# Kernel optimization log

Hardware: AMD Instinct MI355X
Metric: run time of the kernel (lower is better)

Reference implementation:

```python
import jax, jax.numpy as jnp
import numpy as np

B, N, D, H, DH, E, BIAS_DIM = 8, 512, 512, 8, 64, 32768, 8

def setup_inputs() -> dict:
    key = jax.random.key(0)
    ks = jax.random.split(key, 10)
    states = jax.random.normal(ks[0], (B, N, D), jnp.float32)
    key_states = jax.random.normal(ks[1], (B, N, D), jnp.float32)
    # causal mask, broadcastable over heads: [B,1,N,N]
    masks = jnp.broadcast_to(jnp.tril(jnp.ones((N, N), jnp.float32)), (B, 1, N, N))
    edge_type = jax.random.randint(ks[2], (E, 1), 0, BIAS_DIM, jnp.int32)
    b_idx = jax.random.randint(ks[3], (E, 1), 0, B, jnp.int32)
    q_idx = jax.random.randint(ks[4], (E, 1), 0, N, jnp.int32)
    k_idx = jax.random.randint(ks[5], (E, 1), 0, N, jnp.int32)
    attention_bias = jnp.concatenate([edge_type, b_idx, q_idx, k_idx], axis=1)
    s = 0.05
    Wq = jax.random.normal(ks[6], (D, H, DH), jnp.float32) * s
    Wk = jax.random.normal(ks[7], (D, H, DH), jnp.float32) * s
    Wv = jax.random.normal(ks[8], (D, H, DH), jnp.float32) * s
    k2 = jax.random.split(ks[9], 3)
    Wo = jax.random.normal(k2[0], (H, DH, D), jnp.float32) * s
    bias_embs = jax.random.normal(k2[1], (BIAS_DIM, DH), jnp.float32) * s
    bias_scalar = jax.random.normal(k2[2], (DH, 1), jnp.float32) * s
    return {"states": states, "key_states": key_states, "masks": masks,
            "attention_bias": attention_bias, "Wq": Wq, "Wk": Wk, "Wv": Wv,
            "Wo": Wo, "bias_embs": bias_embs, "bias_scalar": bias_scalar}

def reference(states, key_states, masks, attention_bias, Wq, Wk, Wv, Wo, bias_embs, bias_scalar):
    q = jnp.einsum('btd,dha->btha', states, Wq)
    k = jnp.einsum('btd,dha->btha', key_states, Wk)
    v = jnp.einsum('btd,dha->btha', key_states, Wv)
    alpha = jnp.einsum('bkha,bqha->bhqk', k, q)  # [B,H,Q,K]
    # sparse edge bias: embed edge types, project to scalar, scatter into [B,Q,K]
    et = attention_bias[:, 0]
    bias_vals = (bias_embs[et] @ bias_scalar)[:, 0]  # [E]
    bq, bk = alpha.shape[2], alpha.shape[3]
    bias_mat = jnp.zeros((alpha.shape[0], bq, bk), alpha.dtype)
    bias_mat = bias_mat.at[attention_bias[:, 1], attention_bias[:, 2], attention_bias[:, 3]].add(bias_vals)
    summed_keys = jnp.sum(k, axis=-1)  # [B,K,H]
    alpha = alpha + jnp.einsum('bqk,bkh->bhqk', bias_mat, summed_keys)
    alpha = alpha * jax.lax.rsqrt(jnp.float32(DH))
    neg = jnp.finfo(jnp.float32).min
    alpha = alpha * masks + (1.0 - jnp.ceil(masks)) * neg
    alpha = jax.nn.softmax(alpha, axis=-1)
    alpha = alpha * masks
    context = jnp.einsum('bhqk,bkha->bqha', alpha, v)
    return jnp.einsum('btha,had->btd', context, Wo)
```

## Files before the change

### kernel.cpp

```cpp
#include <hip/hip_runtime.h>

typedef unsigned short u16;
typedef unsigned int u32;
typedef __bf16 bf16x8 __attribute__((ext_vector_type(8)));
typedef float f32x4 __attribute__((ext_vector_type(4)));
typedef u16 u16x8 __attribute__((ext_vector_type(8)));
typedef u16 u16x4 __attribute__((ext_vector_type(4)));


__device__ __forceinline__ u16 f2b(float f) {
  union { float f; u32 i; } v; v.f = f;
  u32 r = v.i + 0x7fffu + ((v.i >> 16) & 1u);
  return (u16)(r >> 16);
}
__device__ __forceinline__ float b2f(u16 u) {
  union { u32 i; float f; } v; v.i = ((u32)u) << 16; return v.f;
}

#define GLL16(gp, lp)                                                      \
  __builtin_amdgcn_global_load_lds(                                       \
      (const __attribute__((address_space(1))) u32*)(gp),                 \
      (__attribute__((address_space(3))) u32*)(lp), 16, 0, 0)

__device__ __forceinline__ void stage64(const u16* g, u16* l, int wave, int lane) {
  int rsub = lane >> 3;
  int gs = (((lane & 7) ^ rsub) << 3);
  #pragma unroll
  for (int c = 0; c < 2; c++) {
    int ch = wave * 2 + c;
    GLL16(g + (size_t)(ch * 8 + rsub) * 512 + gs, l + ch * 512);
  }
}
__device__ __forceinline__ void stage128(const u16* g, u16* l, int wave, int lane) {
  int rsub = lane >> 3;
  int gs = (((lane & 7) ^ rsub) << 3);
  #pragma unroll
  for (int c = 0; c < 4; c++) {
    int ch = wave * 4 + c;
    GLL16(g + (size_t)(ch * 8 + rsub) * 512 + gs, l + ch * 512);
  }
}
__device__ __forceinline__ int swz(int row, int g) {
  return row * 64 + ((g ^ (row & 7)) << 3);
}

__global__ __launch_bounds__(256) void prologue(
    const float* __restrict__ states, const float* __restrict__ key_states,
    const float* __restrict__ Wq, const float* __restrict__ Wk,
    const float* __restrict__ Wv, const float* __restrict__ Wo,
    const int* __restrict__ ab, const float* __restrict__ be,
    const float* __restrict__ bsc,
    u16* __restrict__ sb, u16* __restrict__ kbin, u16* __restrict__ wbase,
    float* __restrict__ bias_mat, int n_edges) {
  __shared__ u16 t[32][33];
  __shared__ float tv[8];
  int bid = blockIdx.x;
  int tid = threadIdx.x;
  if (bid < 2048) {
    const float* src = (bid >= 1024) ? key_states : states;
    u16* dst = (bid >= 1024) ? kbin : sb;
    int gid = (bid & 1023) * 256 + tid;
    const float4* sp = (const float4*)src + (size_t)gid * 2;
    float4 x0 = sp[0], x1 = sp[1];
    u16x8 p;
    p[0] = f2b(x0.x); p[1] = f2b(x0.y); p[2] = f2b(x0.z); p[3] = f2b(x0.w);
    p[4] = f2b(x1.x); p[5] = f2b(x1.y); p[6] = f2b(x1.z); p[7] = f2b(x1.w);
    *(u16x8*)(dst + (size_t)gid * 8) = p;
  } else if (bid < 3072) {
    int tt = bid - 2048;
    int z = tt >> 8, rem = tt & 255;
    int bx = rem & 15, by = rem >> 4;
    const float* src; float sc = 1.f;
    if (z == 0)      { src = Wq; sc = 0.125f; }
    else if (z == 1) { src = Wk; }
    else if (z == 2) { src = Wv; }
    else             { src = Wo; }
    u16* dst = wbase + (size_t)z * 262144;
    int tx = tid & 31, ty = tid >> 5;
    int c0 = bx * 32, r0 = by * 32;
    #pragma unroll
    for (int i = ty; i < 32; i += 8) t[i][tx] = f2b(src[(r0 + i) * 512 + c0 + tx] * sc);
    __syncthreads();
    #pragma unroll
    for (int i = ty; i < 32; i += 8) dst[(c0 + i) * 512 + r0 + tx] = t[tx][i];
  } else {
    if (tid < 8) {
      float s = 0.f;
      #pragma unroll
      for (int a = 0; a < 64; a++) s += be[tid * 64 + a] * bsc[a];
      tv[tid] = s * 0.125f;
    }
    __syncthreads();
    int e = (bid - 3072) * 256 + tid;
    if (e < n_edges) {
      int et = ab[e * 4 + 0];
      int b  = ab[e * 4 + 1];
      int qi = ab[e * 4 + 2];
      int ki = ab[e * 4 + 3];
      atomicAdd(&bias_mat[((size_t)b * 512 + qi) * 512 + ki], tv[et]);
    }
  }
}

__global__ __launch_bounds__(256) void qkv_gemm(const u16* __restrict__ sb,
                                                const u16* __restrict__ kbin,
                                                const u16* __restrict__ wT,
                                                u16* __restrict__ qb,
                                                u16* __restrict__ kbo,
                                                u16* __restrict__ vtb,
                                                float* __restrict__ summed) {
  __shared__ alignas(16) u16 As[2][64 * 64];
  __shared__ alignas(16) u16 Bs[2][128 * 64];
  __shared__ float ssum[4][64];
  int tid = threadIdx.x;
  int lane = tid & 63, wave = tid >> 6;
  int quad = lane >> 4, ln = lane & 15;
  int row0 = blockIdx.x * 64;
  int col0 = blockIdx.y * 128;
  const u16* A = (col0 < 512) ? sb : kbin;
  const u16* Ab = A + (size_t)row0 * 512;
  const u16* Bb = wT + (size_t)col0 * 512;

  f32x4 acc[4][2];
  #pragma unroll
  for (int i = 0; i < 4; i++)
    #pragma unroll
    for (int j = 0; j < 2; j++) acc[i][j] = (f32x4){0.f, 0.f, 0.f, 0.f};

  stage64(Ab, As[0], wave, lane);
  stage128(Bb, Bs[0], wave, lane);

  int cur = 0;
  for (int k0 = 0; k0 < 512; k0 += 64) {
    __syncthreads();
    if (k0 < 448) {
      stage64(Ab + k0 + 64, As[cur ^ 1], wave, lane);
      stage128(Bb + k0 + 64, Bs[cur ^ 1], wave, lane);
    }
    #pragma unroll
    for (int s = 0; s < 2; s++) {
      bf16x8 af[4], bfv[2];
      #pragma unroll
      for (int i = 0; i < 4; i++)
        af[i] = *(bf16x8*)&As[cur][swz(i * 16 + ln, s * 4 + quad)];
      #pragma unroll
      for (int j = 0; j < 2; j++)
        bfv[j] = *(bf16x8*)&Bs[cur][swz(wave * 32 + j * 16 + ln, s * 4 + quad)];
      #pragma unroll
      for (int i = 0; i < 4; i++)
        #pragma unroll
        for (int j = 0; j < 2; j++)
          acc[i][j] = __builtin_amdgcn_mfma_f32_16x16x32_bf16(af[i], bfv[j], acc[i][j], 0, 0, 0);
    }
    cur ^= 1;
  }

  int region = col0 >> 9;
  int nbase = col0 & 511;
  if (region <= 1) {
    u16* Cout = region ? kbo : qb;
    #pragma unroll
    for (int i = 0; i < 4; i++)
      #pragma unroll
      for (int j = 0; j < 2; j++) {
        int mb = row0 + i * 16 + quad * 4;
        int n = nbase + wave * 32 + j * 16 + ln;
        #pragma unroll
        for (int r = 0; r < 4; r++)
          Cout[(size_t)(mb + r) * 512 + n] = f2b(acc[i][j][r]);
      }
    if (region == 1) {
      #pragma unroll
      for (int i = 0; i < 4; i++)
        #pragma unroll
        for (int r = 0; r < 4; r++) {
          float v = acc[i][0][r] + acc[i][1][r];
          v += __shfl_xor(v, 1);
          v += __shfl_xor(v, 2);
          v += __shfl_xor(v, 4);
          v += __shfl_xor(v, 8);
          if (ln == 0) ssum[wave][i * 16 + quad * 4 + r] = v;
        }
      __syncthreads();
      if (tid < 128) {
        int hl = tid >> 6, row = tid & 63;
        float s = ssum[hl * 2][row] + ssum[hl * 2 + 1][row];
        int m = row0 + row;
        int b = m >> 9, t = m & 511;
        int h = (nbase >> 6) + hl;
        summed[((size_t)(b * 8 + h)) * 512 + t] = s;
      }
    }
  } else {
    #pragma unroll
    for (int i = 0; i < 4; i++)
      #pragma unroll
      for (int j = 0; j < 2; j++) {
        int mb = row0 + i * 16 + quad * 4;
        int bb = mb >> 9, t0 = mb & 511;
        int a_abs = nbase + wave * 32 + j * 16 + ln;
        int h = a_abs >> 6, a = a_abs & 63;
        u16x4 p;
        p[0] = f2b(acc[i][j][0]); p[1] = f2b(acc[i][j][1]);
        p[2] = f2b(acc[i][j][2]); p[3] = f2b(acc[i][j][3]);
        *(u16x4*)&vtb[(((size_t)bb * 8 + h) * 64 + a) * 512 + t0] = p;
      }
  }
}

__global__ __launch_bounds__(256) void out_gemm(const u16* __restrict__ A,
                                                const u16* __restrict__ BT,
                                                float* __restrict__ C) {
  __shared__ alignas(16) u16 As[2][64 * 64];
  __shared__ alignas(16) u16 Bs[2][64 * 64];
  int tid = threadIdx.x;
  int lane = tid & 63, wave = tid >> 6;
  int quad = lane >> 4, ln = lane & 15;
  int wr = wave >> 1, wc = wave & 1;
  int row0 = blockIdx.x * 64;
  int col0 = blockIdx.y * 64;
  const u16* Ab = A + (size_t)row0 * 512;
  const u16* Bb = BT + (size_t)col0 * 512;

  f32x4 acc[2][2];
  #pragma unroll
  for (int i = 0; i < 2; i++)
    #pragma unroll
    for (int j = 0; j < 2; j++) acc[i][j] = (f32x4){0.f, 0.f, 0.f, 0.f};

  stage64(Ab, As[0], wave, lane);
  stage64(Bb, Bs[0], wave, lane);

  int cur = 0;
  for (int k0 = 0; k0 < 512; k0 += 64) {
    __syncthreads();
    if (k0 < 448) {
      stage64(Ab + k0 + 64, As[cur ^ 1], wave, lane);
      stage64(Bb + k0 + 64, Bs[cur ^ 1], wave, lane);
    }
    #pragma unroll
    for (int s = 0; s < 2; s++) {
      bf16x8 af[2], bfv[2];
      #pragma unroll
      for (int i = 0; i < 2; i++)
        af[i] = *(bf16x8*)&As[cur][swz(wr * 32 + i * 16 + ln, s * 4 + quad)];
      #pragma unroll
      for (int j = 0; j < 2; j++)
        bfv[j] = *(bf16x8*)&Bs[cur][swz(wc * 32 + j * 16 + ln, s * 4 + quad)];
      #pragma unroll
      for (int i = 0; i < 2; i++)
        #pragma unroll
        for (int j = 0; j < 2; j++)
          acc[i][j] = __builtin_amdgcn_mfma_f32_16x16x32_bf16(af[i], bfv[j], acc[i][j], 0, 0, 0);
    }
    cur ^= 1;
  }
  #pragma unroll
  for (int i = 0; i < 2; i++)
    #pragma unroll
    for (int j = 0; j < 2; j++) {
      int mb = row0 + wr * 32 + i * 16 + quad * 4;
      int n = col0 + wc * 32 + j * 16 + ln;
      #pragma unroll
      for (int r = 0; r < 4; r++)
        C[(size_t)(mb + r) * 512 + n] = acc[i][j][r];
    }
}

__global__ __launch_bounds__(256) void attn_mfma(const u16* __restrict__ q,
                                                 const u16* __restrict__ k,
                                                 const u16* __restrict__ vt,
                                                 const float* __restrict__ bias_mat,
                                                 const float* __restrict__ summed,
                                                 u16* __restrict__ ctx,
                                                 float* __restrict__ Opart,
                                                 float* __restrict__ ml) {
  __shared__ alignas(16) u16 Qs[64 * 64];
  __shared__ alignas(16) u16 Ks[2][64 * 64];
  __shared__ alignas(16) u16 Vs[2][64 * 64];
  __shared__ alignas(16) u16 Ps[4][16 * 72];
  int tid = threadIdx.x;
  int wave = tid >> 6, lane = tid & 63;
  int quad = lane >> 4, ln = lane & 15;
  int p2 = blockIdx.x;
  int bh, u;
  {
    const int fours[6] = {3, 4, 6, 8, 10, 11};
    const int threes[2] = {2, 9};
    const int ones[2] = {0, 5};
    const int twos[2] = {1, 7};
    if (p2 < 384)      { bh = p2 & 63; u = fours[p2 >> 6]; }
    else if (p2 < 512) { int q2 = p2 - 384; bh = q2 & 63; u = threes[q2 >> 6]; }
    else if (p2 < 640) { int q2 = p2 - 512; bh = q2 & 63; u = ones[q2 >> 6]; }
    else               { int q2 = p2 - 640; bh = q2 & 63; u = twos[q2 >> 6]; }
  }
  int b = bh >> 3, h = bh & 7;
  int qt, kb0, kbe, part = 0;
  bool partial;
  if (u < 4) { qt = u; kb0 = 0; kbe = u; partial = false; }
  else {
    int v = u - 4; qt = 4 + (v >> 1); part = v & 1; partial = true;
    if (part == 0) { kb0 = 0; kbe = 3; } else { kb0 = 4; kbe = qt; }
  }
  int q0 = qt * 64;

  const u16* qb_ = q + ((size_t)(b * 512 + q0)) * 512 + h * 64;
  const u16* kb_ = k + ((size_t)(b * 512)) * 512 + h * 64;
  const u16* vb_ = vt + ((size_t)bh * 64) * 512;

  stage64(qb_, Qs, wave, lane);
  stage64(kb_ + (size_t)kb0 * 64 * 512, Ks[0], wave, lane);
  stage64(vb_ + kb0 * 64, Vs[0], wave, lane);

  float m_r[4], l_r[4];
  f32x4 o[4];
  #pragma unroll
  for (int r = 0; r < 4; r++) { m_r[r] = -3.40282347e38f; l_r[r] = 0.f; }
  #pragma unroll
  for (int nt = 0; nt < 4; nt++) o[nt] = (f32x4){0.f, 0.f, 0.f, 0.f};

  int qrow = q0 + wave * 16 + quad * 4;

  float c_skv[4], c_bias[4][4];
  #pragma unroll
  for (int nt = 0; nt < 4; nt++) {
    int t = kb0 * 64 + nt * 16 + ln;
    c_skv[nt] = summed[bh * 512 + t];
    const float* bp2 = bias_mat + ((size_t)(b * 512 + qrow)) * 512 + t;
    #pragma unroll
    for (int r = 0; r < 4; r++) c_bias[nt][r] = bp2[(size_t)r * 512];
  }

  int cur = 0;
  for (int kb = kb0; kb <= kbe; kb++) {
    __syncthreads();

    float n_skv[4], n_bias[4][4];
    if (kb < kbe) {
      stage64(kb_ + (size_t)(kb + 1) * 64 * 512, Ks[cur ^ 1], wave, lane);
      stage64(vb_ + (kb + 1) * 64, Vs[cur ^ 1], wave, lane);
      #pragma unroll
      for (int nt = 0; nt < 4; nt++) {
        int t = (kb + 1) * 64 + nt * 16 + ln;
        n_skv[nt] = summed[bh * 512 + t];
        const float* bp2 = bias_mat + ((size_t)(b * 512 + qrow)) * 512 + t;
        #pragma unroll
        for (int r = 0; r < 4; r++) n_bias[nt][r] = bp2[(size_t)r * 512];
      }
    }

    bf16x8 aq0 = *(bf16x8*)&Qs[swz(wave * 16 + ln, quad)];
    bf16x8 aq1 = *(bf16x8*)&Qs[swz(wave * 16 + ln, 4 + quad)];
    f32x4 s[4];
    #pragma unroll
    for (int nt = 0; nt < 4; nt++) {
      bf16x8 b0 = *(bf16x8*)&Ks[cur][swz(nt * 16 + ln, quad)];
      bf16x8 b1 = *(bf16x8*)&Ks[cur][swz(nt * 16 + ln, 4 + quad)];
      s[nt] = (f32x4){0.f, 0.f, 0.f, 0.f};
      s[nt] = __builtin_amdgcn_mfma_f32_16x16x32_bf16(aq0, b0, s[nt], 0, 0, 0);
      s[nt] = __builtin_amdgcn_mfma_f32_16x16x32_bf16(aq1, b1, s[nt], 0, 0, 0);
    }

    #pragma unroll
    for (int nt = 0; nt < 4; nt++) {
      int t = kb * 64 + nt * 16 + ln;
      #pragma unroll
      for (int r = 0; r < 4; r++) {
        float val = s[nt][r] + c_bias[nt][r] * c_skv[nt];
        s[nt][r] = (t <= qrow + r) ? val : -3.40282347e38f;
      }
    }

    float alpha[4];
    #pragma unroll
    for (int r = 0; r < 4; r++) {
      float tm = fmaxf(fmaxf(s[0][r], s[1][r]), fmaxf(s[2][r], s[3][r]));
      #pragma unroll
      for (int off = 8; off; off >>= 1) tm = fmaxf(tm, __shfl_xor(tm, off));
      float mn = fmaxf(m_r[r], tm);
      alpha[r] = __expf(m_r[r] - mn);
      m_r[r] = mn;
      float rs = 0.f;
      #pragma unroll
      for (int nt = 0; nt < 4; nt++) {
        float pp = __expf(s[nt][r] - mn);
        s[nt][r] = pp;
        rs += pp;
      }
      #pragma unroll
      for (int off = 8; off; off >>= 1) rs += __shfl_xor(rs, off);
      l_r[r] = l_r[r] * alpha[r] + rs;
    }

    #pragma unroll
    for (int nt = 0; nt < 4; nt++)
      #pragma unroll
      for (int r = 0; r < 4; r++)
        Ps[wave][(quad * 4 + r) * 72 + nt * 16 + ln] = f2b(s[nt][r]);
    #pragma unroll
    for (int nt = 0; nt < 4; nt++)
      #pragma unroll
      for (int r = 0; r < 4; r++)
        o[nt][r] *= alpha[r];

    bf16x8 ap0 = *(bf16x8*)&Ps[wave][ln * 72 + quad * 8];
    bf16x8 ap1 = *(bf16x8*)&Ps[wave][ln * 72 + 32 + quad * 8];
    #pragma unroll
    for (int nt = 0; nt < 4; nt++) {
      bf16x8 b0 = *(bf16x8*)&Vs[cur][swz(nt * 16 + ln, quad)];
      bf16x8 b1 = *(bf16x8*)&Vs[cur][swz(nt * 16 + ln, 4 + quad)];
      o[nt] = __builtin_amdgcn_mfma_f32_16x16x32_bf16(ap0, b0, o[nt], 0, 0, 0);
      o[nt] = __builtin_amdgcn_mfma_f32_16x16x32_bf16(ap1, b1, o[nt], 0, 0, 0);
    }

    if (kb < kbe) {
      #pragma unroll
      for (int nt = 0; nt < 4; nt++) {
        c_skv[nt] = n_skv[nt];
        #pragma unroll
        for (int r = 0; r < 4; r++) c_bias[nt][r] = n_bias[nt][r];
      }
    }
    cur ^= 1;
  }

  if (!partial) {
    #pragma unroll
    for (int r = 0; r < 4; r++) {
      float inv = 1.f / l_r[r];
      int qr2 = qrow + r;
      u16* dst = ctx + ((size_t)(b * 512 + qr2)) * 512 + h * 64;
      #pragma unroll
      for (int nt = 0; nt < 4; nt++)
        dst[nt * 16 + ln] = f2b(o[nt][r] * inv);
    }
  } else {
    #pragma unroll
    for (int r = 0; r < 4; r++) {
      int row = qrow + r - 256;
      float* dst = Opart + (((size_t)(part * 64 + bh)) * 256 + row) * 64;
      #pragma unroll
      for (int nt = 0; nt < 4; nt++)
        dst[nt * 16 + ln] = o[nt][r];
    }
    if (ln == 0) {
      #pragma unroll
      for (int r = 0; r < 4; r++) {
        int row = qrow + r - 256;
        float* mp = ml + (((size_t)(part * 64 + bh)) * 256 + row) * 2;
        mp[0] = m_r[r];
        mp[1] = l_r[r];
      }
    }
  }
}

__global__ __launch_bounds__(256) void attn_merge(const float* __restrict__ Opart,
                                                  const float* __restrict__ ml,
                                                  u16* __restrict__ ctx) {
  int gid = blockIdx.x * 256 + threadIdx.x;
  int col = gid & 63;
  int row = (gid >> 6) & 255;
  int bh = gid >> 14;
  size_t i0 = (size_t)bh * 256 + row;
  size_t i1 = (size_t)(64 + bh) * 256 + row;
  float m0 = ml[i0 * 2], l0 = ml[i0 * 2 + 1];
  float m1 = ml[i1 * 2], l1 = ml[i1 * 2 + 1];
  float m = fmaxf(m0, m1);
  float a0 = __expf(m0 - m), a1 = __expf(m1 - m);
  float l = l0 * a0 + l1 * a1;
  float O0 = Opart[i0 * 64 + col], O1 = Opart[i1 * 64 + col];
  float val = (O0 * a0 + O1 * a1) / l;
  int b = bh >> 3, h = bh & 7, qrow = 256 + row;
  ctx[((size_t)(b * 512 + qrow)) * 512 + h * 64 + col] = f2b(val);
}

extern "C" void kernel_launch(void* const* d_in, const int* in_sizes, int n_in,
                              void* d_out, int out_size, void* d_ws, size_t ws_size,
                              hipStream_t stream) {
  const float* states     = (const float*)d_in[0];
  const float* key_states = (const float*)d_in[1];
  const int*   ab         = (const int*)d_in[3];
  const float* Wq         = (const float*)d_in[4];
  const float* Wk         = (const float*)d_in[5];
  const float* Wv         = (const float*)d_in[6];
  const float* Wo         = (const float*)d_in[7];
  const float* be         = (const float*)d_in[8];
  const float* bsc        = (const float*)d_in[9];
  float* out = (float*)d_out;

  char* ws = (char*)d_ws;
  const size_t MB = 1024 * 1024;
  u16* wbase    = (u16*)(ws);
  u16* wot      = (u16*)(ws + 1536 * 1024);
  u16* sb       = (u16*)(ws + 2 * MB);
  u16* kbin     = (u16*)(ws + 6 * MB);
  u16* qb       = (u16*)(ws + 10 * MB);
  u16* kbo      = (u16*)(ws + 14 * MB);
  u16* vtb      = (u16*)(ws + 18 * MB);
  u16* ctxb     = (u16*)(ws + 22 * MB);
  float* bias_m = (float*)(ws + 26 * MB);
  float* summed = (float*)(ws + 34 * MB);
  float* Opart  = (float*)(ws + 35 * MB);
  float* mlbuf  = (float*)(ws + 43 * MB);

  int n_edges = in_sizes[3] / 4;

  hipMemsetAsync(bias_m, 0, (size_t)8 * MB, stream);
  prologue<<<dim3(3072 + (n_edges + 255) / 256), 256, 0, stream>>>(
      states, key_states, Wq, Wk, Wv, Wo, ab, be, bsc, sb, kbin, wbase, bias_m, n_edges);
  qkv_gemm<<<dim3(64, 12), 256, 0, stream>>>(sb, kbin, wbase, qb, kbo, vtb, summed);
  attn_mfma<<<dim3(768), 256, 0, stream>>>(qb, kbo, vtb, bias_m, summed, ctxb, Opart, mlbuf);
  attn_merge<<<dim3(4096), 256, 0, stream>>>(Opart, mlbuf, ctxb);
  out_gemm<<<dim3(64, 8), 256, 0, stream>>>(ctxb, wot, out);
}
```

Measured before the change: 134.6 us.

## Fuse all stages into one persistent cooperative kernel with grid syncs

Replaces the memset plus five separate kernel launches with a single cooperative persistent kernel. Stages are separated by grid-wide barriers and use a shared-memory union. The bias zeroing and per-edge bias scalar computation move inside the kernel, and the edge scatter is deferred until after the barrier. This removes launch gaps and inter-kernel drain, at the cost of grid-sync overhead, grid-stride loops bounded by occupancy, and a larger shared-memory footprint that may lower occupancy.

```diff
diff --git a/kernel.cpp b/kernel.cpp
--- a/kernel.cpp
+++ b/kernel.cpp
@@ -1,4 +1,7 @@
 #include <hip/hip_runtime.h>
+#include <hip/hip_cooperative_groups.h>
+
+namespace cg = cooperative_groups;
 
 typedef unsigned short u16;
 typedef unsigned int u32;
@@ -12,9 +15,6 @@
   union { float f; u32 i; } v; v.f = f;
   u32 r = v.i + 0x7fffu + ((v.i >> 16) & 1u);
   return (u16)(r >> 16);
-}
-__device__ __forceinline__ float b2f(u16 u) {
-  union { u32 i; float f; } v; v.i = ((u32)u) << 16; return v.f;
 }
 
 #define GLL16(gp, lp)                                                      \
@@ -44,435 +44,439 @@
   return row * 64 + ((g ^ (row & 7)) << 3);
 }
 
-__global__ __launch_bounds__(256) void prologue(
+__global__ __launch_bounds__(256) void fused(
     const float* __restrict__ states, const float* __restrict__ key_states,
-    const float* __restrict__ Wq, const float* __restrict__ Wk,
-    const float* __restrict__ Wv, const float* __restrict__ Wo,
-    const int* __restrict__ ab, const float* __restrict__ be,
+    const int* __restrict__ ab, const float* __restrict__ Wq,
+    const float* __restrict__ Wk, const float* __restrict__ Wv,
+    const float* __restrict__ Wo, const float* __restrict__ be,
     const float* __restrict__ bsc,
     u16* __restrict__ sb, u16* __restrict__ kbin, u16* __restrict__ wbase,
-    float* __restrict__ bias_mat, int n_edges) {
-  __shared__ u16 t[32][33];
-  __shared__ float tv[8];
+    float* __restrict__ bias_m, float* __restrict__ summed,
+    u16* __restrict__ qb, u16* __restrict__ kbo, u16* __restrict__ vtb,
+    u16* __restrict__ ctxb, float* __restrict__ Opart, float* __restrict__ mlbuf,
+    float* __restrict__ out, int n_edges) {
+  __shared__ alignas(16) union SM {
+    u16 t[32][33];
+    struct {
+      alignas(16) u16 As[2][64 * 64];
+      alignas(16) u16 Bs[2][128 * 64];
+      float ssum[4][64];
+    } g1;
+    struct {
+      alignas(16) u16 Qs[64 * 64];
+      alignas(16) u16 Ks[2][64 * 64];
+      alignas(16) u16 Vs[2][64 * 64];
+      alignas(16) u16 Ps[4][16 * 72];
+    } at;
+    struct {
+      alignas(16) u16 As[2][64 * 64];
+      alignas(16) u16 Bs[2][64 * 64];
+    } g2;
+  } sm;
+
+  cg::grid_group gg = cg::this_grid();
+
+  int tid = threadIdx.x;
   int bid = blockIdx.x;
-  int tid = threadIdx.x;
-  if (bid < 2048) {
-    const float* src = (bid >= 1024) ? key_states : states;
-    u16* dst = (bid >= 1024) ? kbin : sb;
-    int gid = (bid & 1023) * 256 + tid;
-    const float4* sp = (const float4*)src + (size_t)gid * 2;
-    float4 x0 = sp[0], x1 = sp[1];
-    u16x8 p;
-    p[0] = f2b(x0.x); p[1] = f2b(x0.y); p[2] = f2b(x0.z); p[3] = f2b(x0.w);
-    p[4] = f2b(x1.x); p[5] = f2b(x1.y); p[6] = f2b(x1.z); p[7] = f2b(x1.w);
-    *(u16x8*)(dst + (size_t)gid * 8) = p;
-  } else if (bid < 3072) {
-    int tt = bid - 2048;
-    int z = tt >> 8, rem = tt & 255;
-    int bx = rem & 15, by = rem >> 4;
-    const float* src; float sc = 1.f;
-    if (z == 0)      { src = Wq; sc = 0.125f; }
-    else if (z == 1) { src = Wk; }
-    else if (z == 2) { src = Wv; }
-    else             { src = Wo; }
-    u16* dst = wbase + (size_t)z * 262144;
+  const int G = gridDim.x;
+  const int gsz = G << 8;
+  int gtid = bid * 256 + tid;
+  int lane = tid & 63, wave = tid >> 6;
+  int quad = lane >> 4, ln = lane & 15;
+
+  {
+    float4 z4 = {0.f, 0.f, 0.f, 0.f};
+    for (int i = gtid; i < 524288; i += gsz) ((float4*)bias_m)[i] = z4;
+
+    for (int c = gtid; c < 524288; c += gsz) {
+      const float* src = (c < 262144) ? states : key_states;
+      u16* dst = (c < 262144) ? sb : kbin;
+      int g = c & 262143;
+      const float4* sp = (const float4*)src + (size_t)g * 2;
+      float4 x0 = sp[0], x1 = sp[1];
+      u16x8 p;
+      p[0] = f2b(x0.x); p[1] = f2b(x0.y); p[2] = f2b(x0.z); p[3] = f2b(x0.w);
+      p[4] = f2b(x1.x); p[5] = f2b(x1.y); p[6] = f2b(x1.z); p[7] = f2b(x1.w);
+      *(u16x8*)(dst + (size_t)g * 8) = p;
+    }
+
     int tx = tid & 31, ty = tid >> 5;
-    int c0 = bx * 32, r0 = by * 32;
-    #pragma unroll
-    for (int i = ty; i < 32; i += 8) t[i][tx] = f2b(src[(r0 + i) * 512 + c0 + tx] * sc);
-    __syncthreads();
-    #pragma unroll
-    for (int i = ty; i < 32; i += 8) dst[(c0 + i) * 512 + r0 + tx] = t[tx][i];
-  } else {
-    if (tid < 8) {
-      float s = 0.f;
-      #pragma unroll
-      for (int a = 0; a < 64; a++) s += be[tid * 64 + a] * bsc[a];
-      tv[tid] = s * 0.125f;
-    }
-    __syncthreads();
-    int e = (bid - 3072) * 256 + tid;
-    if (e < n_edges) {
+    for (int tt = bid; tt < 1024; tt += G) {
+      int z = tt >> 8, rem = tt & 255;
+      int bx = rem & 15, by = rem >> 4;
+      const float* src; float sc = 1.f;
+      if (z == 0)      { src = Wq; sc = 0.125f; }
+      else if (z == 1) { src = Wk; }
+      else if (z == 2) { src = Wv; }
+      else             { src = Wo; }
+      u16* dst = wbase + (size_t)z * 262144;
+      int c0 = bx * 32, r0 = by * 32;
+      #pragma unroll
+      for (int i = ty; i < 32; i += 8) sm.t[i][tx] = f2b(src[(r0 + i) * 512 + c0 + tx] * sc);
+      __syncthreads();
+      #pragma unroll
+      for (int i = ty; i < 32; i += 8) dst[(c0 + i) * 512 + r0 + tx] = sm.t[tx][i];
+      __syncthreads();
+    }
+  }
+  gg.sync();
+
+  {
+    for (int e = gtid; e < n_edges; e += gsz) {
       int et = ab[e * 4 + 0];
       int b  = ab[e * 4 + 1];
       int qi = ab[e * 4 + 2];
       int ki = ab[e * 4 + 3];
-      atomicAdd(&bias_mat[((size_t)b * 512 + qi) * 512 + ki], tv[et]);
-    }
-  }
-}
-
-__global__ __launch_bounds__(256) void qkv_gemm(const u16* __restrict__ sb,
-                                                const u16* __restrict__ kbin,
-                                                const u16* __restrict__ wT,
-                                                u16* __restrict__ qb,
-                                                u16* __restrict__ kbo,
-                                                u16* __restrict__ vtb,
-                                                float* __restrict__ summed) {
-  __shared__ alignas(16) u16 As[2][64 * 64];
-  __shared__ alignas(16) u16 Bs[2][128 * 64];
-  __shared__ float ssum[4][64];
-  int tid = threadIdx.x;
-  int lane = tid & 63, wave = tid >> 6;
-  int quad = lane >> 4, ln = lane & 15;
-  int row0 = blockIdx.x * 64;
-  int col0 = blockIdx.y * 128;
-  const u16* A = (col0 < 512) ? sb : kbin;
-  const u16* Ab = A + (size_t)row0 * 512;
-  const u16* Bb = wT + (size_t)col0 * 512;
-
-  f32x4 acc[4][2];
-  #pragma unroll
-  for (int i = 0; i < 4; i++)
+      float s = 0.f;
+      #pragma unroll 8
+      for (int a = 0; a < 64; a++) s += be[et * 64 + a] * bsc[a];
+      atomicAdd(&bias_m[((size_t)b * 512 + qi) * 512 + ki], s * 0.125f);
+    }
+
+    for (int vb = bid; vb < 768; vb += G) {
+      __syncthreads();
+      int bx = vb & 63, by = vb >> 6;
+      int row0 = bx * 64;
+      int col0 = by * 128;
+      const u16* A = (col0 < 512) ? sb : kbin;
+      const u16* Ab = A + (size_t)row0 * 512;
+      const u16* Bb = wbase + (size_t)col0 * 512;
+
+      f32x4 acc[4][2];
+      #pragma unroll
+      for (int i = 0; i < 4; i++)
+        #pragma unroll
+        for (int j = 0; j < 2; j++) acc[i][j] = (f32x4){0.f, 0.f, 0.f, 0.f};
+
+      stage64(Ab, sm.g1.As[0], wave, lane);
+      stage128(Bb, sm.g1.Bs[0], wave, lane);
+
+      int cur = 0;
+      for (int k0 = 0; k0 < 512; k0 += 64) {
+        __syncthreads();
+        if (k0 < 448) {
+          stage64(Ab + k0 + 64, sm.g1.As[cur ^ 1], wave, lane);
+          stage128(Bb + k0 + 64, sm.g1.Bs[cur ^ 1], wave, lane);
+        }
+        #pragma unroll
+        for (int s = 0; s < 2; s++) {
+          bf16x8 af[4], bfv[2];
+          #pragma unroll
+          for (int i = 0; i < 4; i++)
+            af[i] = *(bf16x8*)&sm.g1.As[cur][swz(i * 16 + ln, s * 4 + quad)];
+          #pragma unroll
+          for (int j = 0; j < 2; j++)
+            bfv[j] = *(bf16x8*)&sm.g1.Bs[cur][swz(wave * 32 + j * 16 + ln, s * 4 + quad)];
+          #pragma unroll
+          for (int i = 0; i < 4; i++)
+            #pragma unroll
+            for (int j = 0; j < 2; j++)
+              acc[i][j] = __builtin_amdgcn_mfma_f32_16x16x32_bf16(af[i], bfv[j], acc[i][j], 0, 0, 0);
+        }
+        cur ^= 1;
+      }
+
+      int region = col0 >> 9;
+      int nbase = col0 & 511;
+      if (region <= 1) {
+        u16* Cout = region ? kbo : qb;
+        #pragma unroll
+        for (int i = 0; i < 4; i++)
+          #pragma unroll
+          for (int j = 0; j < 2; j++) {
+            int mb = row0 + i * 16 + quad * 4;
+            int n = nbase + wave * 32 + j * 16 + ln;
+            #pragma unroll
+            for (int r = 0; r < 4; r++)
+              Cout[(size_t)(mb + r) * 512 + n] = f2b(acc[i][j][r]);
+          }
+        if (region == 1) {
+          #pragma unroll
+          for (int i = 0; i < 4; i++)
+            #pragma unroll
+            for (int r = 0; r < 4; r++) {
+              float v = acc[i][0][r] + acc[i][1][r];
+              v += __shfl_xor(v, 1);
+              v += __shfl_xor(v, 2);
+              v += __shfl_xor(v, 4);
+              v += __shfl_xor(v, 8);
+              if (ln == 0) sm.g1.ssum[wave][i * 16 + quad * 4 + r] = v;
+            }
+          __syncthreads();
+          if (tid < 128) {
+            int hl = tid >> 6, row = tid & 63;
+            float s = sm.g1.ssum[hl * 2][row] + sm.g1.ssum[hl * 2 + 1][row];
+            int m = row0 + row;
+            int b = m >> 9, t = m & 511;
+            int h = (nbase >> 6) + hl;
+            summed[((size_t)(b * 8 + h)) * 512 + t] = s;
+          }
+        }
+      } else {
+        #pragma unroll
+        for (int i = 0; i < 4; i++)
+          #pragma unroll
+          for (int j = 0; j < 2; j++) {
+            int mb = row0 + i * 16 + quad * 4;
+            int bb = mb >> 9, t0 = mb & 511;
+            int a_abs = nbase + wave * 32 + j * 16 + ln;
+            int h = a_abs >> 6, a = a_abs & 63;
+            u16x4 p;
+            p[0] = f2b(acc[i][j][0]); p[1] = f2b(acc[i][j][1]);
+            p[2] = f2b(acc[i][j][2]); p[3] = f2b(acc[i][j][3]);
+            *(u16x4*)&vtb[(((size_t)bb * 8 + h) * 64 + a) * 512 + t0] = p;
+          }
+      }
+    }
+  }
+  gg.sync();
+
+  for (int vb = bid; vb < 768; vb += G) {
+    __syncthreads();
+    int p2 = vb;
+    int bh, u;
+    {
+      const int fours[6] = {3, 4, 6, 8, 10, 11};
+      const int threes[2] = {2, 9};
+      const int ones[2] = {0, 5};
+      const int twos[2] = {1, 7};
+      if (p2 < 384)      { bh = p2 & 63; u = fours[p2 >> 6]; }
+      else if (p2 < 512) { int q2 = p2 - 384; bh = q2 & 63; u = threes[q2 >> 6]; }
+      else if (p2 < 640) { int q2 = p2 - 512; bh = q2 & 63; u = ones[q2 >> 6]; }
+      else               { int q2 = p2 - 640; bh = q2 & 63; u = twos[q2 >> 6]; }
+    }
+    int b = bh >> 3, h = bh & 7;
+    int qt, kb0, kbe, part = 0;
+    bool partial;
+    if (u < 4) { qt = u; kb0 = 0; kbe = u; partial = false; }
+    else {
+      int v = u - 4; qt = 4 + (v >> 1); part = v & 1; partial = true;
+      if (part == 0) { kb0 = 0; kbe = 3; } else { kb0 = 4; kbe = qt; }
+    }
+    int q0 = qt * 64;
+
+    const u16* qb_ = qb + ((size_t)(b * 512 + q0)) * 512 + h * 64;
+    const u16* kb_ = kbo + ((size_t)(b * 512)) * 512 + h * 64;
+    const u16* vb_ = vtb + ((size_t)bh * 64) * 512;
+
+    stage64(qb_, sm.at.Qs, wave, lane);
+    stage64(kb_ + (size_t)kb0 * 64 * 512, sm.at.Ks[0], wave, lane);
+    stage64(vb_ + kb0 * 64, sm.at.Vs[0], wave, lane);
+
+    float m_r[4], l_r[4];
+    f32x4 o[4];
     #pragma unroll
-    for (int j = 0; j < 2; j++) acc[i][j] = (f32x4){0.f, 0.f, 0.f, 0.f};
-
-  stage64(Ab, As[0], wave, lane);
-  stage128(Bb, Bs[0], wave, lane);
-
-  int cur = 0;
-  for (int k0 = 0; k0 < 512; k0 += 64) {
-    __syncthreads();
-    if (k0 < 448) {
-      stage64(Ab + k0 + 64, As[cur ^ 1], wave, lane);
-      stage128(Bb + k0 + 64, Bs[cur ^ 1], wave, lane);
-    }
+    for (int r = 0; r < 4; r++) { m_r[r] = -3.40282347e38f; l_r[r] = 0.f; }
     #pragma unroll
-    for (int s = 0; s < 2; s++) {
-      bf16x8 af[4], bfv[2];
-      #pragma unroll
-      for (int i = 0; i < 4; i++)
-        af[i] = *(bf16x8*)&As[cur][swz(i * 16 + ln, s * 4 + quad)];
-      #pragma unroll
-      for (int j = 0; j < 2; j++)
-        bfv[j] = *(bf16x8*)&Bs[cur][swz(wave * 32 + j * 16 + ln, s * 4 + quad)];
-      #pragma unroll
-      for (int i = 0; i < 4; i++)
-        #pragma unroll
-        for (int j = 0; j < 2; j++)
-          acc[i][j] = __builtin_amdgcn_mfma_f32_16x16x32_bf16(af[i], bfv[j], acc[i][j], 0, 0, 0);
-    }
-    cur ^= 1;
-  }
-
-  int region = col0 >> 9;
-  int nbase = col0 & 511;
-  if (region <= 1) {
-    u16* Cout = region ? kbo : qb;
-    #pragma unroll
-    for (int i = 0; i < 4; i++)
-      #pragma unroll
-      for (int j = 0; j < 2; j++) {
-        int mb = row0 + i * 16 + quad * 4;
-        int n = nbase + wave * 32 + j * 16 + ln;
-        #pragma unroll
-        for (int r = 0; r < 4; r++)
-          Cout[(size_t)(mb + r) * 512 + n] = f2b(acc[i][j][r]);
-      }
-    if (region == 1) {
-      #pragma unroll
-      for (int i = 0; i < 4; i++)
-        #pragma unroll
-        for (int r = 0; r < 4; r++) {
-          float v = acc[i][0][r] + acc[i][1][r];
-          v += __shfl_xor(v, 1);
-          v += __shfl_xor(v, 2);
-          v += __shfl_xor(v, 4);
-          v += __shfl_xor(v, 8);
-          if (ln == 0) ssum[wave][i * 16 + quad * 4 + r] = v;
-        }
-      __syncthreads();
-      if (tid < 128) {
-        int hl = tid >> 6, row = tid & 63;
-        float s = ssum[hl * 2][row] + ssum[hl * 2 + 1][row];
-        int m = row0 + row;
-        int b = m >> 9, t = m & 511;
-        int h = (nbase >> 6) + hl;
-        summed[((size_t)(b * 8 + h)) * 512 + t] = s;
-      }
-    }
-  } else {
-    #pragma unroll
-    for (int i = 0; i < 4; i++)
-      #pragma unroll
-      for (int j = 0; j < 2; j++) {
-        int mb = row0 + i * 16 + quad * 4;
-        int bb = mb >> 9, t0 = mb & 511;
-        int a_abs = nbase + wave * 32 + j * 16 + ln;
-        int h = a_abs >> 6, a = a_abs & 63;
-        u16x4 p;
-        p[0] = f2b(acc[i][j][0]); p[1] = f2b(acc[i][j][1]);
-        p[2] = f2b(acc[i][j][2]); p[3] = f2b(acc[i][j][3]);
-        *(u16x4*)&vtb[(((size_t)bb * 8 + h) * 64 + a) * 512 + t0] = p;
-      }
-  }
-}
-
-__global__ __launch_bounds__(256) void out_gemm(const u16* __restrict__ A,
-                                                const u16* __restrict__ BT,
-                                                float* __restrict__ C) {
-  __shared__ alignas(16) u16 As[2][64 * 64];
-  __shared__ alignas(16) u16 Bs[2][64 * 64];
-  int tid = threadIdx.x;
-  int lane = tid & 63, wave = tid >> 6;
-  int quad = lane >> 4, ln = lane & 15;
-  int wr = wave >> 1, wc = wave & 1;
-  int row0 = blockIdx.x * 64;
-  int col0 = blockIdx.y * 64;
-  const u16* Ab = A + (size_t)row0 * 512;
-  const u16* Bb = BT + (size_t)col0 * 512;
-
-  f32x4 acc[2][2];
-  #pragma unroll
-  for (int i = 0; i < 2; i++)
-    #pragma unroll
-    for (int j = 0; j < 2; j++) acc[i][j] = (f32x4){0.f, 0.f, 0.f, 0.f};
-
-  stage64(Ab, As[0], wave, lane);
-  stage64(Bb, Bs[0], wave, lane);
-
-  int cur = 0;
-  for (int k0 = 0; k0 < 512; k0 += 64) {
-    __syncthreads();
-    if (k0 < 448) {
-      stage64(Ab + k0 + 64, As[cur ^ 1], wave, lane);
-      stage64(Bb + k0 + 64, Bs[cur ^ 1], wave, lane);
-    }
-    #pragma unroll
-    for (int s = 0; s < 2; s++) {
-      bf16x8 af[2], bfv[2];
-      #pragma unroll
-      for (int i = 0; i < 2; i++)
-        af[i] = *(bf16x8*)&As[cur][swz(wr * 32 + i * 16 + ln, s * 4 + quad)];
-      #pragma unroll
-      for (int j = 0; j < 2; j++)
-        bfv[j] = *(bf16x8*)&Bs[cur][swz(wc * 32 + j * 16 + ln, s * 4 + quad)];
-      #pragma unroll
-      for (int i = 0; i < 2; i++)
-        #pragma unroll
-        for (int j = 0; j < 2; j++)
-          acc[i][j] = __builtin_amdgcn_mfma_f32_16x16x32_bf16(af[i], bfv[j], acc[i][j], 0, 0, 0);
-    }
-    cur ^= 1;
-  }
-  #pragma unroll
-  for (int i = 0; i < 2; i++)
-    #pragma unroll
-    for (int j = 0; j < 2; j++) {
-      int mb = row0 + wr * 32 + i * 16 + quad * 4;
-      int n = col0 + wc * 32 + j * 16 + ln;
-      #pragma unroll
-      for (int r = 0; r < 4; r++)
-        C[(size_t)(mb + r) * 512 + n] = acc[i][j][r];
-    }
-}
-
-__global__ __launch_bounds__(256) void attn_mfma(const u16* __restrict__ q,
-                                                 const u16* __restrict__ k,
-                                                 const u16* __restrict__ vt,
-                                                 const float* __restrict__ bias_mat,
-                                                 const float* __restrict__ summed,
-                                                 u16* __restrict__ ctx,
-                                                 float* __restrict__ Opart,
-                                                 float* __restrict__ ml) {
-  __shared__ alignas(16) u16 Qs[64 * 64];
-  __shared__ alignas(16) u16 Ks[2][64 * 64];
-  __shared__ alignas(16) u16 Vs[2][64 * 64];
-  __shared__ alignas(16) u16 Ps[4][16 * 72];
-  int tid = threadIdx.x;
-  int wave = tid >> 6, lane = tid & 63;
-  int quad = lane >> 4, ln = lane & 15;
-  int p2 = blockIdx.x;
-  int bh, u;
-  {
-    const int fours[6] = {3, 4, 6, 8, 10, 11};
-    const int threes[2] = {2, 9};
-    const int ones[2] = {0, 5};
-    const int twos[2] = {1, 7};
-    if (p2 < 384)      { bh = p2 & 63; u = fours[p2 >> 6]; }
-    else if (p2 < 512) { int q2 = p2 - 384; bh = q2 & 63; u = threes[q2 >> 6]; }
-    else if (p2 < 640) { int q2 = p2 - 512; bh = q2 & 63; u = ones[q2 >> 6]; }
-    else               { int q2 = p2 - 640; bh = q2 & 63; u = twos[q2 >> 6]; }
-  }
-  int b = bh >> 3, h = bh & 7;
-  int qt, kb0, kbe, part = 0;
-  bool partial;
-  if (u < 4) { qt = u; kb0 = 0; kbe = u; partial = false; }
-  else {
-    int v = u - 4; qt = 4 + (v >> 1); part = v & 1; partial = true;
-    if (part == 0) { kb0 = 0; kbe = 3; } else { kb0 = 4; kbe = qt; }
-  }
-  int q0 = qt * 64;
-
-  const u16* qb_ = q + ((size_t)(b * 512 + q0)) * 512 + h * 64;
-  const u16* kb_ = k + ((size_t)(b * 512)) * 512 + h * 64;
-  const u16* vb_ = vt + ((size_t)bh * 64) * 512;
-
-  stage64(qb_, Qs, wave, lane);
-  stage64(kb_ + (size_t)kb0 * 64 * 512, Ks[0], wave, lane);
-  stage64(vb_ + kb0 * 64, Vs[0], wave, lane);
-
-  float m_r[4], l_r[4];
-  f32x4 o[4];
-  #pragma unroll
-  for (int r = 0; r < 4; r++) { m_r[r] = -3.40282347e38f; l_r[r] = 0.f; }
-  #pragma unroll
-  for (int nt = 0; nt < 4; nt++) o[nt] = (f32x4){0.f, 0.f, 0.f, 0.f};
-
-  int qrow = q0 + wave * 16 + quad * 4;
-
-  float c_skv[4], c_bias[4][4];
-  #pragma unroll
-  for (int nt = 0; nt < 4; nt++) {
-    int t = kb0 * 64 + nt * 16 + ln;
-    c_skv[nt] = summed[bh * 512 + t];
-    const float* bp2 = bias_mat + ((size_t)(b * 512 + qrow)) * 512 + t;
-    #pragma unroll
-    for (int r = 0; r < 4; r++) c_bias[nt][r] = bp2[(size_t)r * 512];
-  }
-
-  int cur = 0;
-  for (int kb = kb0; kb <= kbe; kb++) {
-    __syncthreads();
-
-    float n_skv[4], n_bias[4][4];
-    if (kb < kbe) {
-      stage64(kb_ + (size_t)(kb + 1) * 64 * 512, Ks[cur ^ 1], wave, lane);
-      stage64(vb_ + (kb + 1) * 64, Vs[cur ^ 1], wave, lane);
-      #pragma unroll
-      for (int nt = 0; nt < 4; nt++) {
-        int t = (kb + 1) * 64 + nt * 16 + ln;
-        n_skv[nt] = summed[bh * 512 + t];
-        const float* bp2 = bias_mat + ((size_t)(b * 512 + qrow)) * 512 + t;
-        #pragma unroll
-        for (int r = 0; r < 4; r++) n_bias[nt][r] = bp2[(size_t)r * 512];
-      }
-    }
-
-    bf16x8 aq0 = *(bf16x8*)&Qs[swz(wave * 16 + ln, quad)];
-    bf16x8 aq1 = *(bf16x8*)&Qs[swz(wave * 16 + ln, 4 + quad)];
-    f32x4 s[4];
+    for (int nt = 0; nt < 4; nt++) o[nt] = (f32x4){0.f, 0.f, 0.f, 0.f};
+
+    int qrow = q0 + wave * 16 + quad * 4;
+
+    float c_skv[4], c_bias[4][4];
     #pragma unroll
     for (int nt = 0; nt < 4; nt++) {
-      bf16x8 b0 = *(bf16x8*)&Ks[cur][swz(nt * 16 + ln, quad)];
-      bf16x8 b1 = *(bf16x8*)&Ks[cur][swz(nt * 16 + ln, 4 + quad)];
-      s[nt] = (f32x4){0.f, 0.f, 0.f, 0.f};
-      s[nt] = __builtin_amdgcn_mfma_f32_16x16x32_bf16(aq0, b0, s[nt], 0, 0, 0);
-      s[nt] = __builtin_amdgcn_mfma_f32_16x16x32_bf16(aq1, b1, s[nt], 0, 0, 0);
-    }
-
-    #pragma unroll
-    for (int nt = 0; nt < 4; nt++) {
-      int t = kb * 64 + nt * 16 + ln;
+      int t = kb0 * 64 + nt * 16 + ln;
+      c_skv[nt] = summed[bh * 512 + t];
+      const float* bp2 = bias_m + ((size_t)(b * 512 + qrow)) * 512 + t;
+      #pragma unroll
+      for (int r = 0; r < 4; r++) c_bias[nt][r] = bp2[(size_t)r * 512];
+    }
+
+    int cur = 0;
+    for (int kb = kb0; kb <= kbe; kb++) {
+      __syncthreads();
+
+      float n_skv[4], n_bias[4][4];
+      if (kb < kbe) {
+        stage64(kb_ + (size_t)(kb + 1) * 64 * 512, sm.at.Ks[cur ^ 1], wave, lane);
+        stage64(vb_ + (kb + 1) * 64, sm.at.Vs[cur ^ 1], wave, lane);
+        #pragma unroll
+        for (int nt = 0; nt < 4; nt++) {
+          int t = (kb + 1) * 64 + nt * 16 + ln;
+          n_skv[nt] = summed[bh * 512 + t];
+          const float* bp2 = bias_m + ((size_t)(b * 512 + qrow)) * 512 + t;
+          #pragma unroll
+          for (int r = 0; r < 4; r++) n_bias[nt][r] = bp2[(size_t)r * 512];
+        }
+      }
+
+      bf16x8 aq0 = *(bf16x8*)&sm.at.Qs[swz(wave * 16 + ln, quad)];
+      bf16x8 aq1 = *(bf16x8*)&sm.at.Qs[swz(wave * 16 + ln, 4 + quad)];
+      f32x4 s[4];
+      #pragma unroll
+      for (int nt = 0; nt < 4; nt++) {
+        bf16x8 b0 = *(bf16x8*)&sm.at.Ks[cur][swz(nt * 16 + ln, quad)];
+        bf16x8 b1 = *(bf16x8*)&sm.at.Ks[cur][swz(nt * 16 + ln, 4 + quad)];
+        s[nt] = (f32x4){0.f, 0.f, 0.f, 0.f};
+        s[nt] = __builtin_amdgcn_mfma_f32_16x16x32_bf16(aq0, b0, s[nt], 0, 0, 0);
+        s[nt] = __builtin_amdgcn_mfma_f32_16x16x32_bf16(aq1, b1, s[nt], 0, 0, 0);
+      }
+
+      #pragma unroll
+      for (int nt = 0; nt < 4; nt++) {
+        int t = kb * 64 + nt * 16 + ln;
+        #pragma unroll
+        for (int r = 0; r < 4; r++) {
+          float val = s[nt][r] + c_bias[nt][r] * c_skv[nt];
+          s[nt][r] = (t <= qrow + r) ? val : -3.40282347e38f;
+        }
+      }
+
+      float alpha[4];
       #pragma unroll
       for (int r = 0; r < 4; r++) {
-        float val = s[nt][r] + c_bias[nt][r] * c_skv[nt];
-        s[nt][r] = (t <= qrow + r) ? val : -3.40282347e38f;
-      }
-    }
-
-    float alpha[4];
-    #pragma unroll
-    for (int r = 0; r < 4; r++) {
-      float tm = fmaxf(fmaxf(s[0][r], s[1][r]), fmaxf(s[2][r], s[3][r]));
-      #pragma unroll
-      for (int off = 8; off; off >>= 1) tm = fmaxf(tm, __shfl_xor(tm, off));
-      float mn = fmaxf(m_r[r], tm);
-      alpha[r] = __expf(m_r[r] - mn);
-      m_r[r] = mn;
-      float rs = 0.f;
+        float tm = fmaxf(fmaxf(s[0][r], s[1][r]), fmaxf(s[2][r], s[3][r]));
+        #pragma unroll
+        for (int off = 8; off; off >>= 1) tm = fmaxf(tm, __shfl_xor(tm, off));
+        float mn = fmaxf(m_r[r], tm);
+        alpha[r] = __expf(m_r[r] - mn);
+        m_r[r] = mn;
+        float rs = 0.f;
+        #pragma unroll
+        for (int nt = 0; nt < 4; nt++) {
+          float pp = __expf(s[nt][r] - mn);
+          s[nt][r] = pp;
+          rs += pp;
+        }
+        #pragma unroll
+        for (int off = 8; off; off >>= 1) rs += __shfl_xor(rs, off);
+        l_r[r] = l_r[r] * alpha[r] + rs;
+      }
+
+      #pragma unroll
+      for (int nt = 0; nt < 4; nt++)
+        #pragma unroll
+        for (int r = 0; r < 4; r++)
+          sm.at.Ps[wave][(quad * 4 + r) * 72 + nt * 16 + ln] = f2b(s[nt][r]);
+      #pragma unroll
+      for (int nt = 0; nt < 4; nt++)
+        #pragma unroll
+        for (int r = 0; r < 4; r++)
+          o[nt][r] *= alpha[r];
+
+      bf16x8 ap0 = *(bf16x8*)&sm.at.Ps[wave][ln * 72 + quad * 8];
+      bf16x8 ap1 = *(bf16x8*)&sm.at.Ps[wave][ln * 72 + 32 + quad * 8];
       #pragma unroll
       for (int nt = 0; nt < 4; nt++) {
-        float pp = __expf(s[nt][r] - mn);
-        s[nt][r] = pp;
-        rs += pp;
-      }
-      #pragma unroll
-      for (int off = 8; off; off >>= 1) rs += __shfl_xor(rs, off);
-      l_r[r] = l_r[r] * alpha[r] + rs;
-    }
-
-    #pragma unroll
-    for (int nt = 0; nt < 4; nt++)
-      #pragma unroll
-      for (int r = 0; r < 4; r++)
-        Ps[wave][(quad * 4 + r) * 72 + nt * 16 + ln] = f2b(s[nt][r]);
-    #pragma unroll
-    for (int nt = 0; nt < 4; nt++)
-      #pragma unroll
-      for (int r = 0; r < 4; r++)
-        o[nt][r] *= alpha[r];
-
-    bf16x8 ap0 = *(bf16x8*)&Ps[wave][ln * 72 + quad * 8];
-    bf16x8 ap1 = *(bf16x8*)&Ps[wave][ln * 72 + 32 + quad * 8];
-    #pragma unroll
-    for (int nt = 0; nt < 4; nt++) {
-      bf16x8 b0 = *(bf16x8*)&Vs[cur][swz(nt * 16 + ln, quad)];
-      bf16x8 b1 = *(bf16x8*)&Vs[cur][swz(nt * 16 + ln, 4 + quad)];
-      o[nt] = __builtin_amdgcn_mfma_f32_16x16x32_bf16(ap0, b0, o[nt], 0, 0, 0);
-      o[nt] = __builtin_amdgcn_mfma_f32_16x16x32_bf16(ap1, b1, o[nt], 0, 0, 0);
-    }
-
-    if (kb < kbe) {
-      #pragma unroll
-      for (int nt = 0; nt < 4; nt++) {
-        c_skv[nt] = n_skv[nt];
-        #pragma unroll
-        for (int r = 0; r < 4; r++) c_bias[nt][r] = n_bias[nt][r];
-      }
-    }
-    cur ^= 1;
-  }
-
-  if (!partial) {
-    #pragma unroll
-    for (int r = 0; r < 4; r++) {
-      float inv = 1.f / l_r[r];
-      int qr2 = qrow + r;
-      u16* dst = ctx + ((size_t)(b * 512 + qr2)) * 512 + h * 64;
-      #pragma unroll
-      for (int nt = 0; nt < 4; nt++)
-        dst[nt * 16 + ln] = f2b(o[nt][r] * inv);
-    }
-  } else {
-    #pragma unroll
-    for (int r = 0; r < 4; r++) {
-      int row = qrow + r - 256;
-      float* dst = Opart + (((size_t)(part * 64 + bh)) * 256 + row) * 64;
-      #pragma unroll
-      for (int nt = 0; nt < 4; nt++)
-        dst[nt * 16 + ln] = o[nt][r];
-    }
-    if (ln == 0) {
+        bf16x8 b0 = *(bf16x8*)&sm.at.Vs[cur][swz(nt * 16 + ln, quad)];
+        bf16x8 b1 = *(bf16x8*)&sm.at.Vs[cur][swz(nt * 16 + ln, 4 + quad)];
+        o[nt] = __builtin_amdgcn_mfma_f32_16x16x32_bf16(ap0, b0, o[nt], 0, 0, 0);
+        o[nt] = __builtin_amdgcn_mfma_f32_16x16x32_bf16(ap1, b1, o[nt], 0, 0, 0);
+      }
+
+      if (kb < kbe) {
+        #pragma unroll
+        for (int nt = 0; nt < 4; nt++) {
+          c_skv[nt] = n_skv[nt];
+          #pragma unroll
+          for (int r = 0; r < 4; r++) c_bias[nt][r] = n_bias[nt][r];
+        }
+      }
+      cur ^= 1;
+    }
+
+    if (!partial) {
+      #pragma unroll
+      for (int r = 0; r < 4; r++) {
+        float inv = 1.f / l_r[r];
+        int qr2 = qrow + r;
+        u16* dst = ctxb + ((size_t)(b * 512 + qr2)) * 512 + h * 64;
+        #pragma unroll
+        for (int nt = 0; nt < 4; nt++)
+          dst[nt * 16 + ln] = f2b(o[nt][r] * inv);
+      }
+    } else {
       #pragma unroll
       for (int r = 0; r < 4; r++) {
         int row = qrow + r - 256;
-        float* mp = ml + (((size_t)(part * 64 + bh)) * 256 + row) * 2;
-        mp[0] = m_r[r];
-        mp[1] = l_r[r];
-      }
-    }
-  }
-}
-
-__global__ __launch_bounds__(256) void attn_merge(const float* __restrict__ Opart,
-                                                  const float* __restrict__ ml,
-                                                  u16* __restrict__ ctx) {
-  int gid = blockIdx.x * 256 + threadIdx.x;
-  int col = gid & 63;
-  int row = (gid >> 6) & 255;
-  int bh = gid >> 14;
-  size_t i0 = (size_t)bh * 256 + row;
-  size_t i1 = (size_t)(64 + bh) * 256 + row;
-  float m0 = ml[i0 * 2], l0 = ml[i0 * 2 + 1];
-  float m1 = ml[i1 * 2], l1 = ml[i1 * 2 + 1];
-  float m = fmaxf(m0, m1);
-  float a0 = __expf(m0 - m), a1 = __expf(m1 - m);
-  float l = l0 * a0 + l1 * a1;
-  float O0 = Opart[i0 * 64 + col], O1 = Opart[i1 * 64 + col];
-  float val = (O0 * a0 + O1 * a1) / l;
-  int b = bh >> 3, h = bh & 7, qrow = 256 + row;
-  ctx[((size_t)(b * 512 + qrow)) * 512 + h * 64 + col] = f2b(val);
+        float* dst = Opart + (((size_t)(part * 64 + bh)) * 256 + row) * 64;
+        #pragma unroll
+        for (int nt = 0; nt < 4; nt++)
+          dst[nt * 16 + ln] = o[nt][r];
+      }
+      if (ln == 0) {
+        #pragma unroll
+        for (int r = 0; r < 4; r++) {
+          int row = qrow + r - 256;
+          float* mp = mlbuf + (((size_t)(part * 64 + bh)) * 256 + row) * 2;
+          mp[0] = m_r[r];
+          mp[1] = l_r[r];
+        }
+      }
+    }
+  }
+  gg.sync();
+
+  for (int gid = gtid; gid < 1048576; gid += gsz) {
+    int col = gid & 63;
+    int row = (gid >> 6) & 255;
+    int bh = gid >> 14;
+    size_t i0 = (size_t)bh * 256 + row;
+    size_t i1 = (size_t)(64 + bh) * 256 + row;
+    float m0 = mlbuf[i0 * 2], l0 = mlbuf[i0 * 2 + 1];
+    float m1 = mlbuf[i1 * 2], l1 = mlbuf[i1 * 2 + 1];
+    float m = fmaxf(m0, m1);
+    float a0 = __expf(m0 - m), a1 = __expf(m1 - m);
+    float l = l0 * a0 + l1 * a1;
+    float O0 = Opart[i0 * 64 + col], O1 = Opart[i1 * 64 + col];
+    float val = (O0 * a0 + O1 * a1) / l;
+    int b = bh >> 3, h = bh & 7, qrow = 256 + row;
+    ctxb[((size_t)(b * 512 + qrow)) * 512 + h * 64 + col] = f2b(val);
+  }
+  gg.sync();
+
+  for (int vb = bid; vb < 512; vb += G) {
+    __syncthreads();
+    int wr = wave >> 1, wc = wave & 1;
+    int row0 = (vb & 63) * 64;
+    int col0 = (vb >> 6) * 64;
+    const u16* Ab = ctxb + (size_t)row0 * 512;
+    const u16* Bb = (wbase + (size_t)3 * 262144) + (size_t)col0 * 512;
+
+    f32x4 acc[2][2];
+    #pragma unroll
+    for (int i = 0; i < 2; i++)
+      #pragma unroll
+      for (int j = 0; j < 2; j++) acc[i][j] = (f32x4){0.f, 0.f, 0.f, 0.f};
+
+    stage64(Ab, sm.g2.As[0], wave, lane);
+    stage64(Bb, sm.g2.Bs[0], wave, lane);
+
+    int cur = 0;
+    for (int k0 = 0; k0 < 512; k0 += 64) {
+      __syncthreads();
+      if (k0 < 448) {
+        stage64(Ab + k0 + 64, sm.g2.As[cur ^ 1], wave, lane);
+        stage64(Bb + k0 + 64, sm.g2.Bs[cur ^ 1], wave, lane);
+      }
+      #pragma unroll
+      for (int s = 0; s < 2; s++) {
+        bf16x8 af[2], bfv[2];
+        #pragma unroll
+        for (int i = 0; i < 2; i++)
+          af[i] = *(bf16x8*)&sm.g2.As[cur][swz(wr * 32 + i * 16 + ln, s * 4 + quad)];
+        #pragma unroll
+        for (int j = 0; j < 2; j++)
+          bfv[j] = *(bf16x8*)&sm.g2.Bs[cur][swz(wc * 32 + j * 16 + ln, s * 4 + quad)];
+        #pragma unroll
+        for (int i = 0; i < 2; i++)
+          #pragma unroll
+          for (int j = 0; j < 2; j++)
+            acc[i][j] = __builtin_amdgcn_mfma_f32_16x16x32_bf16(af[i], bfv[j], acc[i][j], 0, 0, 0);
+      }
+      cur ^= 1;
+    }
+    #pragma unroll
+    for (int i = 0; i < 2; i++)
+      #pragma unroll
+      for (int j = 0; j < 2; j++) {
+        int mb = row0 + wr * 32 + i * 16 + quad * 4;
+        int n = col0 + wc * 32 + j * 16 + ln;
+        #pragma unroll
+        for (int r = 0; r < 4; r++)
+          out[(size_t)(mb + r) * 512 + n] = acc[i][j][r];
+      }
+  }
 }
 
 extern "C" void kernel_launch(void* const* d_in, const int* in_sizes, int n_in,
@@ -492,7 +496,6 @@
   char* ws = (char*)d_ws;
   const size_t MB = 1024 * 1024;
   u16* wbase    = (u16*)(ws);
-  u16* wot      = (u16*)(ws + 1536 * 1024);
   u16* sb       = (u16*)(ws + 2 * MB);
   u16* kbin     = (u16*)(ws + 6 * MB);
   u16* qb       = (u16*)(ws + 10 * MB);
@@ -506,11 +509,26 @@
 
   int n_edges = in_sizes[3] / 4;
 
-  hipMemsetAsync(bias_m, 0, (size_t)8 * MB, stream);
-  prologue<<<dim3(3072 + (n_edges + 255) / 256), 256, 0, stream>>>(
-      states, key_states, Wq, Wk, Wv, Wo, ab, be, bsc, sb, kbin, wbase, bias_m, n_edges);
-  qkv_gemm<<<dim3(64, 12), 256, 0, stream>>>(sb, kbin, wbase, qb, kbo, vtb, summed);
-  attn_mfma<<<dim3(768), 256, 0, stream>>>(qb, kbo, vtb, bias_m, summed, ctxb, Opart, mlbuf);
-  attn_merge<<<dim3(4096), 256, 0, stream>>>(Opart, mlbuf, ctxb);
-  out_gemm<<<dim3(64, 8), 256, 0, stream>>>(ctxb, wot, out);
+  static int G = 0;
+  if (G == 0) {
+    int dev = 0;
+    hipGetDevice(&dev);
+    int nb = 0;
+    hipOccupancyMaxActiveBlocksPerMultiprocessor(&nb, (const void*)fused, 256, 0);
+    int ncu = 0;
+    hipDeviceGetAttribute(&ncu, hipDeviceAttributeMultiprocessorCount, dev);
+    if (nb < 1) nb = 1;
+    if (ncu < 1) ncu = 256;
+    G = nb * ncu;
+    if (G > 768) G = 768;
+  }
+
+  void* args[] = {
+      (void*)&states, (void*)&key_states, (void*)&ab, (void*)&Wq, (void*)&Wk,
+      (void*)&Wv, (void*)&Wo, (void*)&be, (void*)&bsc,
+      (void*)&sb, (void*)&kbin, (void*)&wbase, (void*)&bias_m, (void*)&summed,
+      (void*)&qb, (void*)&kbo, (void*)&vtb, (void*)&ctxb, (void*)&Opart,
+      (void*)&mlbuf, (void*)&out, (void*)&n_edges};
+  hipLaunchCooperativeKernel((const void*)fused, dim3(G), dim3(256), args, 0,
+                             stream);
 }
```

Result: slower. 291.6 us (+116.6%).
